# Kernel tuning notes

Hardware: AMD Instinct MI355X
Metric: run time of the kernel (lower is better)

Reference implementation:

```python
import jax, jax.numpy as jnp
import numpy as np

B, S, D, H = 2, 2048, 1024, 16
HD = D // H


def setup_inputs() -> dict:
    key = jax.random.key(0)
    ks = jax.random.split(key, 9)
    sc = 0.02
    return {
        "x": jax.random.normal(ks[0], (B, S, D), dtype=jnp.float32),
        "qw": jax.random.normal(ks[1], (D, D), dtype=jnp.float32) * sc,
        "qb": jax.random.normal(ks[2], (D,), dtype=jnp.float32) * sc,
        "kw": jax.random.normal(ks[3], (D, D), dtype=jnp.float32) * sc,
        "kb": jax.random.normal(ks[4], (D,), dtype=jnp.float32) * sc,
        "vw": jax.random.normal(ks[5], (D, D), dtype=jnp.float32) * sc,
        "vb": jax.random.normal(ks[6], (D,), dtype=jnp.float32) * sc,
        "ow": jax.random.normal(ks[7], (D, D), dtype=jnp.float32) * sc,
        "ob": jax.random.normal(ks[8], (D,), dtype=jnp.float32) * sc,
    }


def reference(x, qw, qb, kw, kb, vw, vb, ow, ob):
    b, s, d = x.shape
    # projections (torch Linear: x @ W.T + b)
    q = (x @ qw.T + qb).reshape(b, s, H, HD).transpose(0, 2, 1, 3)  # bhsd
    k = (x @ kw.T + kb).reshape(b, s, H, HD).transpose(0, 2, 1, 3)
    v = (x @ vw.T + vb).reshape(b, s, H, HD).transpose(0, 2, 1, 3)
    scale = 1.0 / jnp.sqrt(jnp.float32(HD))
    score = jnp.einsum("bhsd,bhtd->bhst", q, k) * scale  # bhss
    # causal mask: -inf strictly above diagonal
    mask = jnp.triu(jnp.full((s, s), -jnp.inf, dtype=score.dtype), k=1)
    score = jax.nn.softmax(score + mask, axis=-1)
    o = jnp.einsum("bhst,bhtd->bhsd", score, v)
    o = o.transpose(0, 2, 1, 3).reshape(b, s, d)
    return o @ ow.T + ob
```

## Files before the change

kernel.cpp:

```cpp
#include <hip/hip_runtime.h>
#include <hip/hip_bf16.h>
#include <stdint.h>

typedef __bf16 bf16x8 __attribute__((ext_vector_type(8)));
typedef __bf16 bf16x4 __attribute__((ext_vector_type(4)));
typedef float f32x4 __attribute__((ext_vector_type(4)));
typedef unsigned short ushort_t;


__device__ inline ushort_t f2bf(float f) {
  union { float f; uint32_t u; } v; v.f = f;
  uint32_t r = (v.u + 0x7fffu + ((v.u >> 16) & 1u)) >> 16;
  return (ushort_t)r;
}

__device__ inline void gll16(const void* g, void* l) {
  __builtin_amdgcn_global_load_lds((const __attribute__((address_space(1))) void*)g,
                                   (__attribute__((address_space(3))) void*)l, 16, 0, 0);
}

__global__ void cvt_x(const float* __restrict__ in, ushort_t* __restrict__ out) {
  int i = blockIdx.x * blockDim.x + threadIdx.x;
  float4 f = ((const float4*)in)[i];
  union { ushort_t u[4]; uint2 v; } r;
  r.u[0] = f2bf(f.x); r.u[1] = f2bf(f.y); r.u[2] = f2bf(f.z); r.u[3] = f2bf(f.w);
  ((uint2*)out)[i] = r.v;
}
__global__ void cvt_w(const float* __restrict__ a, const float* __restrict__ b,
                      const float* __restrict__ c, const float* __restrict__ d,
                      ushort_t* __restrict__ out) {
  const float* srcs[4] = {a, b, c, d};
  const float* s = srcs[blockIdx.y];
  ushort_t* o = out + (size_t)blockIdx.y * 1048576;
  int i = blockIdx.x * blockDim.x + threadIdx.x;
  float4 f = ((const float4*)s)[i];
  union { ushort_t u[4]; uint2 v; } r;
  r.u[0] = f2bf(f.x); r.u[1] = f2bf(f.y); r.u[2] = f2bf(f.z); r.u[3] = f2bf(f.w);
  ((uint2*)(o))[i] = r.v;
}

#define NKT 16

__device__ inline void stage_half(const ushort_t* __restrict__ g, ushort_t* l, int tid) {
  #pragma unroll
  for (int i = 0; i < 2; i++) {
    int c = tid + i * 512;
    int row = c >> 3;
    int q = (c & 7) ^ (row & 7);
    gll16(g + (size_t)row * 1024 + q * 8, l + c * 8);
  }
}

__global__ __launch_bounds__(512, 2) void qkv_gemm(
    const ushort_t* __restrict__ xb,
    const ushort_t* __restrict__ qwb, const ushort_t* __restrict__ kwb, const ushort_t* __restrict__ vwb,
    const float* __restrict__ qbias, const float* __restrict__ kbias, const float* __restrict__ vbias,
    ushort_t* __restrict__ qo, ushort_t* __restrict__ ko, ushort_t* __restrict__ vto)
{
  const int z = blockIdx.y;
  const int bx = blockIdx.x;
  const float* bias = (z == 0) ? qbias : (z == 1) ? kbias : vbias;
  const ushort_t* Ap;
  const ushort_t* Bp;
  int m0, n0;
  if (z == 2) {
    Ap = vwb; Bp = xb;
    m0 = (bx & 3) * 256;
    n0 = (bx >> 2) * 256;
  } else {
    Ap = xb; Bp = (z == 0) ? qwb : kwb;
    m0 = (bx >> 2) * 256;
    n0 = (bx & 3) * 256;
  }

  __shared__ __align__(16) ushort_t As[2][2][128 * 64];
  __shared__ __align__(16) ushort_t Bs[2][2][128 * 64];

  const int tid = threadIdx.x;
  const int w = tid >> 6;
  const int lane = tid & 63;
  const int ln = lane & 15;
  const int q4 = lane >> 4;
  const int wm = w & 1;
  const int wn = w >> 1;
  const int bh = wn >> 1;
  const int brow0 = (wn & 1) * 64;

  f32x4 acc[8][4];
  #pragma unroll
  for (int i = 0; i < 8; i++)
    #pragma unroll
    for (int j = 0; j < 4; j++) acc[i][j] = f32x4{0.f, 0.f, 0.f, 0.f};

  stage_half(Ap + (size_t)(m0 +   0) * 1024 +  0, &As[0][0][0], tid);
  stage_half(Ap + (size_t)(m0 + 128) * 1024 +  0, &As[0][1][0], tid);
  stage_half(Bp + (size_t)(n0 +   0) * 1024 +  0, &Bs[0][0][0], tid);
  stage_half(Bp + (size_t)(n0 + 128) * 1024 +  0, &Bs[0][1][0], tid);
  stage_half(Bp + (size_t)(n0 +   0) * 1024 + 64, &Bs[1][0][0], tid);
  stage_half(Bp + (size_t)(n0 + 128) * 1024 + 64, &Bs[1][1][0], tid);
  asm volatile("s_waitcnt vmcnt(4)" ::: "memory");
  __builtin_amdgcn_s_barrier();

  const int achk = ln & 7;

  for (int t = 0; t < NKT; ++t) {
    const int buf = t & 1;
    const ushort_t* Abuf = &As[buf][wm][0];
    const ushort_t* Bbuf = &Bs[buf][bh][0];

    bf16x8 a0[4][2], a4[4][2], b0[2][2], b2[2][2];

    #pragma unroll
    for (int m = 0; m < 4; m++)
      #pragma unroll
      for (int ks = 0; ks < 2; ks++)
        a0[m][ks] = *(const bf16x8*)&Abuf[(m * 16 + ln) * 64 + (((ks * 4 + q4) ^ achk) * 8)];
    #pragma unroll
    for (int n = 0; n < 2; n++)
      #pragma unroll
      for (int ks = 0; ks < 2; ks++)
        b0[n][ks] = *(const bf16x8*)&Bbuf[(brow0 + n * 16 + ln) * 64 + (((ks * 4 + q4) ^ achk) * 8)];
    if (t + 1 < NKT)
      stage_half(Ap + (size_t)m0 * 1024 + (t + 1) * 64, &As[(t + 1) & 1][0][0], tid);
    __builtin_amdgcn_s_barrier();
    asm volatile("s_waitcnt lgkmcnt(0)" ::: "memory");
    __builtin_amdgcn_s_setprio(1);
    #pragma unroll
    for (int m = 0; m < 4; m++)
      #pragma unroll
      for (int n = 0; n < 2; n++)
        #pragma unroll
        for (int ks = 0; ks < 2; ks++)
          acc[m][n] = __builtin_amdgcn_mfma_f32_16x16x32_bf16(a0[m][ks], b0[n][ks], acc[m][n], 0, 0, 0);
    __builtin_amdgcn_s_setprio(0);
    __builtin_amdgcn_s_barrier();

    #pragma unroll
    for (int n = 0; n < 2; n++)
      #pragma unroll
      for (int ks = 0; ks < 2; ks++)
        b2[n][ks] = *(const bf16x8*)&Bbuf[(brow0 + (n + 2) * 16 + ln) * 64 + (((ks * 4 + q4) ^ achk) * 8)];
    if (t + 1 < NKT)
      stage_half(Ap + (size_t)(m0 + 128) * 1024 + (t + 1) * 64, &As[(t + 1) & 1][1][0], tid);
    __builtin_amdgcn_s_barrier();
    asm volatile("s_waitcnt lgkmcnt(0)" ::: "memory");
    __builtin_amdgcn_s_setprio(1);
    #pragma unroll
    for (int m = 0; m < 4; m++)
      #pragma unroll
      for (int n = 0; n < 2; n++)
        #pragma unroll
        for (int ks = 0; ks < 2; ks++)
          acc[m][n + 2] = __builtin_amdgcn_mfma_f32_16x16x32_bf16(a0[m][ks], b2[n][ks], acc[m][n + 2], 0, 0, 0);
    __builtin_amdgcn_s_setprio(0);
    __builtin_amdgcn_s_barrier();

    #pragma unroll
    for (int m = 0; m < 4; m++)
      #pragma unroll
      for (int ks = 0; ks < 2; ks++)
        a4[m][ks] = *(const bf16x8*)&Abuf[((m + 4) * 16 + ln) * 64 + (((ks * 4 + q4) ^ achk) * 8)];
    if (t + 2 < NKT)
      stage_half(Bp + (size_t)n0 * 1024 + (t + 2) * 64, &Bs[buf][0][0], tid);
    __builtin_amdgcn_s_barrier();
    asm volatile("s_waitcnt lgkmcnt(0)" ::: "memory");
    __builtin_amdgcn_s_setprio(1);
    #pragma unroll
    for (int m = 0; m < 4; m++)
      #pragma unroll
      for (int n = 0; n < 2; n++)
        #pragma unroll
        for (int ks = 0; ks < 2; ks++)
          acc[m + 4][n + 2] = __builtin_amdgcn_mfma_f32_16x16x32_bf16(a4[m][ks], b2[n][ks], acc[m + 4][n + 2], 0, 0, 0);
    __builtin_amdgcn_s_setprio(0);
    __builtin_amdgcn_s_barrier();

    if (t + 2 < NKT)
      stage_half(Bp + (size_t)(n0 + 128) * 1024 + (t + 2) * 64, &Bs[buf][1][0], tid);
    __builtin_amdgcn_s_barrier();
    __builtin_amdgcn_s_setprio(1);
    #pragma unroll
    for (int m = 0; m < 4; m++)
      #pragma unroll
      for (int n = 0; n < 2; n++)
        #pragma unroll
        for (int ks = 0; ks < 2; ks++)
          acc[m + 4][n] = __builtin_amdgcn_mfma_f32_16x16x32_bf16(a4[m][ks], b0[n][ks], acc[m + 4][n], 0, 0, 0);
    __builtin_amdgcn_s_setprio(0);
    if (t + 2 < NKT) {
      asm volatile("s_waitcnt vmcnt(4)" ::: "memory");
    } else if (t + 1 < NKT) {
      asm volatile("s_waitcnt vmcnt(0)" ::: "memory");
    }
    __builtin_amdgcn_s_barrier();
  }

  if (z == 2) {
    #pragma unroll
    for (int n = 0; n < 4; n++) {
      int col = n0 + wn * 64 + n * 16 + ln;
      int bb = col >> 11, s = col & 2047;
      size_t base = (size_t)bb * 2097152 + s;
      #pragma unroll
      for (int m = 0; m < 8; m++) {
        int prow = m0 + wm * 128 + m * 16 + q4 * 4;
        #pragma unroll
        for (int r = 0; r < 4; r++) {
          int p = prow + r;
          vto[base + (size_t)p * 2048] = f2bf(acc[m][n][r] + bias[p]);
        }
      }
    }
  } else {
    #pragma unroll
    for (int n = 0; n < 4; n++) {
      int col = n0 + wn * 64 + n * 16 + ln;
      float bv = bias[col];
      int h = col >> 6, hd = col & 63;
      #pragma unroll
      for (int m = 0; m < 8; m++) {
        int rowb = m0 + wm * 128 + m * 16 + q4 * 4;
        #pragma unroll
        for (int r = 0; r < 4; r++) {
          int row = rowb + r;
          int b = row >> 11, s = row & 2047;
          float val = acc[m][n][r] + bv;
          if (z == 0) {
            qo[((size_t)((b * 16 + h) * 2048 + s)) * 64 + hd] = f2bf(val * 0.180336884f);
          } else {
            ko[((size_t)((b * 16 + h) * 2048 + s)) * 64 + hd] = f2bf(val);
          }
        }
      }
    }
  }
}

#define PAD 72
#define PPAD 68
__global__ __launch_bounds__(256) void attn(
    const ushort_t* __restrict__ qp, const ushort_t* __restrict__ kp,
    const ushort_t* __restrict__ vtp, ushort_t* __restrict__ op)
{
  __shared__ __align__(16) ushort_t Ks[64 * PAD];
  __shared__ __align__(16) ushort_t Vts[64 * PAD];
  __shared__ __align__(16) ushort_t Ps[8][16 * PPAD];

  const int tid = threadIdx.x;
  const int w = tid >> 6;
  const int lane = tid & 63;
  const int ln = lane & 15;
  const int q4 = lane >> 4;
  const int bh = blockIdx.y;
  const int b = bh >> 4, h = bh & 15;
  int tswz = (blockIdx.x + blockIdx.y) & 15;
  const int qt = (blockIdx.y & 16) ? (15 - tswz) : tswz;
  const int q0 = qt * 128;
  const int nt = 2 * qt + 2;

  const int c0 = tid, c1 = tid + 256;
  const int kr0_row = c0 >> 3, kr0_col = (c0 & 7) * 8;
  const int kr1_row = c1 >> 3, kr1_col = (c1 & 7) * 8;

  bf16x8 onesf;
  {
    union { ushort_t u[8]; bf16x8 v; } t;
    #pragma unroll
    for (int j = 0; j < 8; j++) t.u[j] = 0x3F80;
    onesf = t.v;
  }

  bf16x8 qf[2][2];
  #pragma unroll
  for (int s = 0; s < 2; s++) {
    const ushort_t* base = qp + ((size_t)bh * 2048 + q0 + w * 32 + s * 16 + ln) * 64 + q4 * 8;
    qf[s][0] = *(const bf16x8*)(base);
    qf[s][1] = *(const bf16x8*)(base + 32);
  }

  f32x4 acc_o[2][4];
  f32x4 acc_l[2];
  #pragma unroll
  for (int s = 0; s < 2; s++) {
    acc_l[s] = f32x4{0.f, 0.f, 0.f, 0.f};
    #pragma unroll
    for (int t = 0; t < 4; t++) acc_o[s][t] = f32x4{0.f, 0.f, 0.f, 0.f};
  }

  uint4 kr0, kr1, vr0, vr1;
  {
    const ushort_t* kb = kp + (size_t)bh * 2048 * 64;
    kr0 = *(const uint4*)(kb + kr0_row * 64 + kr0_col);
    kr1 = *(const uint4*)(kb + kr1_row * 64 + kr1_col);
    const ushort_t* vb = vtp + (size_t)bh * 64 * 2048;
    vr0 = *(const uint4*)(vb + (size_t)kr0_row * 2048 + kr0_col);
    vr1 = *(const uint4*)(vb + (size_t)kr1_row * 2048 + kr1_col);
  }

  for (int it = 0; it < nt; it++) {
    if (it) __syncthreads();
    *(uint4*)(&Ks [kr0_row * PAD + kr0_col]) = kr0;
    *(uint4*)(&Ks [kr1_row * PAD + kr1_col]) = kr1;
    *(uint4*)(&Vts[kr0_row * PAD + kr0_col]) = vr0;
    *(uint4*)(&Vts[kr1_row * PAD + kr1_col]) = vr1;
    __syncthreads();

    if (it + 1 < nt) {
      int kv1 = (it + 1) * 64;
      const ushort_t* kb = kp + ((size_t)bh * 2048 + kv1) * 64;
      kr0 = *(const uint4*)(kb + kr0_row * 64 + kr0_col);
      kr1 = *(const uint4*)(kb + kr1_row * 64 + kr1_col);
      const ushort_t* vb = vtp + (size_t)bh * 64 * 2048;
      vr0 = *(const uint4*)(vb + (size_t)kr0_row * 2048 + kv1 + kr0_col);
      vr1 = *(const uint4*)(vb + (size_t)kr1_row * 2048 + kv1 + kr1_col);
    }

    f32x4 sc[2][4];
    #pragma unroll
    for (int s = 0; s < 2; s++)
      #pragma unroll
      for (int t = 0; t < 4; t++) sc[s][t] = f32x4{0.f, 0.f, 0.f, 0.f};
    #pragma unroll
    for (int ks = 0; ks < 2; ks++) {
      bf16x8 kf[4];
      #pragma unroll
      for (int tn = 0; tn < 4; tn++)
        kf[tn] = *(const bf16x8*)(&Ks[(tn * 16 + ln) * PAD + ks * 32 + q4 * 8]);
      #pragma unroll
      for (int s = 0; s < 2; s++)
        #pragma unroll
        for (int tn = 0; tn < 4; tn++)
          sc[s][tn] = __builtin_amdgcn_mfma_f32_16x16x32_bf16(qf[s][ks], kf[tn], sc[s][tn], 0, 0, 0);
    }
    if (it >= 2 * qt) {
      int kv0 = it * 64;
      #pragma unroll
      for (int s = 0; s < 2; s++) {
        int qrow = q0 + w * 32 + s * 16 + q4 * 4;
        #pragma unroll
        for (int tn = 0; tn < 4; tn++) {
          int col = kv0 + tn * 16 + ln;
          #pragma unroll
          for (int r = 0; r < 4; r++)
            if (col > qrow + r) sc[s][tn][r] = -__builtin_inff();
        }
      }
    }
    #pragma unroll
    for (int s = 0; s < 2; s++)
      #pragma unroll
      for (int tn = 0; tn < 4; tn++)
        #pragma unroll
        for (int r = 0; r < 4; r++) {
          float p = __builtin_amdgcn_exp2f(sc[s][tn][r]);
          Ps[w * 2 + s][(q4 * 4 + r) * PPAD + tn * 16 + ln] = (ushort_t)(__float_as_uint(p) >> 16);
        }
    #pragma unroll
    for (int ks = 0; ks < 2; ks++) {
      bf16x8 vf[4];
      #pragma unroll
      for (int tn = 0; tn < 4; tn++)
        vf[tn] = *(const bf16x8*)(&Vts[(tn * 16 + ln) * PAD + ks * 32 + q4 * 8]);
      #pragma unroll
      for (int s = 0; s < 2; s++) {
        const ushort_t* pp = &Ps[w * 2 + s][ln * PPAD + ks * 32 + q4 * 8];
        bf16x4 plo = *(const bf16x4*)(pp);
        bf16x4 phi = *(const bf16x4*)(pp + 4);
        bf16x8 pf = __builtin_shufflevector(plo, phi, 0, 1, 2, 3, 4, 5, 6, 7);
        acc_l[s] = __builtin_amdgcn_mfma_f32_16x16x32_bf16(pf, onesf, acc_l[s], 0, 0, 0);
        #pragma unroll
        for (int tn = 0; tn < 4; tn++)
          acc_o[s][tn] = __builtin_amdgcn_mfma_f32_16x16x32_bf16(pf, vf[tn], acc_o[s][tn], 0, 0, 0);
      }
    }
  }

  #pragma unroll
  for (int s = 0; s < 2; s++) {
    float invl[4];
    #pragma unroll
    for (int r = 0; r < 4; r++) invl[r] = __builtin_amdgcn_rcpf(acc_l[s][r]);
    #pragma unroll
    for (int tn = 0; tn < 4; tn++)
      #pragma unroll
      for (int r = 0; r < 4; r++) {
        int row = q0 + w * 32 + s * 16 + q4 * 4 + r;
        op[((size_t)b * 2048 + row) * 1024 + h * 64 + tn * 16 + ln] =
            f2bf(acc_o[s][tn][r] * invl[r]);
      }
  }
}

__global__ __launch_bounds__(256) void out_gemm(
    const ushort_t* __restrict__ ob_in, const ushort_t* __restrict__ owb,
    const float* __restrict__ obias, float* __restrict__ out)
{
  __shared__ __align__(16) ushort_t As[64 * 64];
  __shared__ __align__(16) ushort_t Bs[128 * 64];

  const int tid = threadIdx.x;
  const int w = tid >> 6;
  const int lane = tid & 63;
  const int ln = lane & 15;
  const int q4 = lane >> 4;
  const int wm = w & 1, wn = w >> 1;
  const int m0 = blockIdx.y * 64;
  const int n0 = blockIdx.x * 128;

  f32x4 acc[2][4];
  #pragma unroll
  for (int i = 0; i < 2; i++)
    #pragma unroll
    for (int j = 0; j < 4; j++) acc[i][j] = f32x4{0.f, 0.f, 0.f, 0.f};

  for (int k0 = 0; k0 < 1024; k0 += 64) {
    __syncthreads();
    #pragma unroll
    for (int i = 0; i < 2; i++) {
      int c = tid + i * 256;
      int row = c >> 3;
      int cq = (c & 7) ^ (row & 7);
      gll16(&ob_in[(size_t)(m0 + row) * 1024 + k0 + cq * 8], &As[c * 8]);
    }
    #pragma unroll
    for (int i = 0; i < 4; i++) {
      int c = tid + i * 256;
      int row = c >> 3;
      int cq = (c & 7) ^ (row & 7);
      gll16(&owb[(size_t)(n0 + row) * 1024 + k0 + cq * 8], &Bs[c * 8]);
    }
    __syncthreads();
    #pragma unroll
    for (int ks = 0; ks < 2; ks++) {
      bf16x8 af[2], bfr[4];
      #pragma unroll
      for (int t = 0; t < 2; t++) {
        int rr = wm * 32 + t * 16 + ln;
        af[t] = *(const bf16x8*)(&As[rr * 64 + (((ks * 4 + q4) ^ (rr & 7)) * 8)]);
      }
      #pragma unroll
      for (int t = 0; t < 4; t++) {
        int rc = wn * 64 + t * 16 + ln;
        bfr[t] = *(const bf16x8*)(&Bs[rc * 64 + (((ks * 4 + q4) ^ (rc & 7)) * 8)]);
      }
      #pragma unroll
      for (int tm = 0; tm < 2; tm++)
        #pragma unroll
        for (int tn = 0; tn < 4; tn++)
          acc[tm][tn] = __builtin_amdgcn_mfma_f32_16x16x32_bf16(af[tm], bfr[tn], acc[tm][tn], 0, 0, 0);
    }
  }

  #pragma unroll
  for (int tn = 0; tn < 4; tn++) {
    int col = n0 + wn * 64 + tn * 16 + ln;
    float bv = obias[col];
    #pragma unroll
    for (int tm = 0; tm < 2; tm++) {
      int rowb = m0 + wm * 32 + tm * 16 + q4 * 4;
      #pragma unroll
      for (int r = 0; r < 4; r++)
        out[(size_t)(rowb + r) * 1024 + col] = acc[tm][tn][r] + bv;
    }
  }
}

extern "C" void kernel_launch(void* const* d_in, const int* in_sizes, int n_in,
                              void* d_out, int out_size, void* d_ws, size_t ws_size,
                              hipStream_t stream) {
  const float* x     = (const float*)d_in[0];
  const float* qw    = (const float*)d_in[1];
  const float* qb    = (const float*)d_in[2];
  const float* kw    = (const float*)d_in[3];
  const float* kb    = (const float*)d_in[4];
  const float* vw    = (const float*)d_in[5];
  const float* vb    = (const float*)d_in[6];
  const float* ow    = (const float*)d_in[7];
  const float* obias = (const float*)d_in[8];
  float* out = (float*)d_out;

  char* ws = (char*)d_ws;
  ushort_t* xb  = (ushort_t*)(ws);
  ushort_t* wb  = (ushort_t*)(ws + 8388608);
  ushort_t* qwb = wb;
  ushort_t* kwb = wb + 1048576;
  ushort_t* vwb = wb + 2097152;
  ushort_t* owb = wb + 3145728;
  ushort_t* qo  = (ushort_t*)(ws + 16777216);
  ushort_t* ko  = (ushort_t*)(ws + 25165824);
  ushort_t* vto = (ushort_t*)(ws + 33554432);
  ushort_t* oo  = (ushort_t*)(ws + 41943040);

  cvt_x<<<dim3(4096), dim3(256), 0, stream>>>(x, xb);
  cvt_w<<<dim3(1024, 4), dim3(256), 0, stream>>>(qw, kw, vw, ow, wb);

  qkv_gemm<<<dim3(64, 3), dim3(512), 0, stream>>>(xb, qwb, kwb, vwb, qb, kb, vb, qo, ko, vto);
  attn<<<dim3(16, 32), dim3(256), 0, stream>>>(qo, ko, vto, oo);
  out_gemm<<<dim3(8, 64), dim3(256), 0, stream>>>(oo, owb, obias, out);
}
```

Measured before the change: 184.9 us.

## Double-buffer attention K/V, keep P in registers, triple-buffer out-projection GEMM

The attention kernel now double-buffers K/V tiles in shared memory with a two-step-ahead register prefetch, so there is one barrier per iteration. It computes scores transposed so the exp'd probabilities can be packed with v_cvt_pk_bf16 and redistributed with ds_bpermute instead of a round trip through an LDS P buffer. MFMA phases are wrapped in s_setprio. The output GEMM gets a 3-stage global_load_lds pipeline with explicit vmcnt waits, which raises LDS use per block and relies on exact outstanding-load counts for correctness.

```diff
diff --git a/kernel.cpp b/kernel.cpp
--- a/kernel.cpp
+++ b/kernel.cpp
@@ -12,6 +12,12 @@
   union { float f; uint32_t u; } v; v.f = f;
   uint32_t r = (v.u + 0x7fffu + ((v.u >> 16) & 1u)) >> 16;
   return (ushort_t)r;
+}
+
+__device__ inline uint32_t cvtpk_bf16(float lo, float hi) {
+  uint32_t r;
+  asm("v_cvt_pk_bf16_f32 %0, %1, %2" : "=v"(r) : "v"(lo), "v"(hi));
+  return r;
 }
 
 __device__ inline void gll16(const void* g, void* l) {
@@ -237,20 +243,21 @@
 }
 
 #define PAD 72
-#define PPAD 68
 __global__ __launch_bounds__(256) void attn(
     const ushort_t* __restrict__ qp, const ushort_t* __restrict__ kp,
     const ushort_t* __restrict__ vtp, ushort_t* __restrict__ op)
 {
-  __shared__ __align__(16) ushort_t Ks[64 * PAD];
-  __shared__ __align__(16) ushort_t Vts[64 * PAD];
-  __shared__ __align__(16) ushort_t Ps[8][16 * PPAD];
+  __shared__ __align__(16) ushort_t Ks[2][64 * PAD];
+  __shared__ __align__(16) ushort_t Vts[2][64 * PAD];
 
   const int tid = threadIdx.x;
   const int w = tid >> 6;
   const int lane = tid & 63;
   const int ln = lane & 15;
   const int q4 = lane >> 4;
+  const bool alo = (q4 < 2);
+  const int psel0 = (((q4 & 1) * 32) + ln) << 2;
+  const int psel1 = psel0 + (16 << 2);
   const int bh = blockIdx.y;
   const int b = bh >> 4, h = bh & 15;
   int tswz = (blockIdx.x + blockIdx.y) & 15;
@@ -287,32 +294,39 @@
     for (int t = 0; t < 4; t++) acc_o[s][t] = f32x4{0.f, 0.f, 0.f, 0.f};
   }
 
+  const ushort_t* kb = kp + (size_t)bh * 2048 * 64;
+  const ushort_t* vb = vtp + (size_t)bh * 64 * 2048;
+
   uint4 kr0, kr1, vr0, vr1;
-  {
-    const ushort_t* kb = kp + (size_t)bh * 2048 * 64;
-    kr0 = *(const uint4*)(kb + kr0_row * 64 + kr0_col);
-    kr1 = *(const uint4*)(kb + kr1_row * 64 + kr1_col);
-    const ushort_t* vb = vtp + (size_t)bh * 64 * 2048;
-    vr0 = *(const uint4*)(vb + (size_t)kr0_row * 2048 + kr0_col);
-    vr1 = *(const uint4*)(vb + (size_t)kr1_row * 2048 + kr1_col);
-  }
+  kr0 = *(const uint4*)(kb + kr0_row * 64 + kr0_col);
+  kr1 = *(const uint4*)(kb + kr1_row * 64 + kr1_col);
+  vr0 = *(const uint4*)(vb + (size_t)kr0_row * 2048 + kr0_col);
+  vr1 = *(const uint4*)(vb + (size_t)kr1_row * 2048 + kr1_col);
+  *(uint4*)(&Ks [0][kr0_row * PAD + kr0_col]) = kr0;
+  *(uint4*)(&Ks [0][kr1_row * PAD + kr1_col]) = kr1;
+  *(uint4*)(&Vts[0][kr0_row * PAD + kr0_col]) = vr0;
+  *(uint4*)(&Vts[0][kr1_row * PAD + kr1_col]) = vr1;
+  kr0 = *(const uint4*)(kb + 64 * 64 + kr0_row * 64 + kr0_col);
+  kr1 = *(const uint4*)(kb + 64 * 64 + kr1_row * 64 + kr1_col);
+  vr0 = *(const uint4*)(vb + (size_t)kr0_row * 2048 + 64 + kr0_col);
+  vr1 = *(const uint4*)(vb + (size_t)kr1_row * 2048 + 64 + kr1_col);
 
   for (int it = 0; it < nt; it++) {
-    if (it) __syncthreads();
-    *(uint4*)(&Ks [kr0_row * PAD + kr0_col]) = kr0;
-    *(uint4*)(&Ks [kr1_row * PAD + kr1_col]) = kr1;
-    *(uint4*)(&Vts[kr0_row * PAD + kr0_col]) = vr0;
-    *(uint4*)(&Vts[kr1_row * PAD + kr1_col]) = vr1;
+    const int cur = it & 1;
     __syncthreads();
-
     if (it + 1 < nt) {
-      int kv1 = (it + 1) * 64;
-      const ushort_t* kb = kp + ((size_t)bh * 2048 + kv1) * 64;
-      kr0 = *(const uint4*)(kb + kr0_row * 64 + kr0_col);
-      kr1 = *(const uint4*)(kb + kr1_row * 64 + kr1_col);
-      const ushort_t* vb = vtp + (size_t)bh * 64 * 2048;
-      vr0 = *(const uint4*)(vb + (size_t)kr0_row * 2048 + kv1 + kr0_col);
-      vr1 = *(const uint4*)(vb + (size_t)kr1_row * 2048 + kv1 + kr1_col);
+      const int nxt = cur ^ 1;
+      *(uint4*)(&Ks [nxt][kr0_row * PAD + kr0_col]) = kr0;
+      *(uint4*)(&Ks [nxt][kr1_row * PAD + kr1_col]) = kr1;
+      *(uint4*)(&Vts[nxt][kr0_row * PAD + kr0_col]) = vr0;
+      *(uint4*)(&Vts[nxt][kr1_row * PAD + kr1_col]) = vr1;
+    }
+    if (it + 2 < nt) {
+      int kv2 = (it + 2) * 64;
+      kr0 = *(const uint4*)(kb + (size_t)kv2 * 64 + kr0_row * 64 + kr0_col);
+      kr1 = *(const uint4*)(kb + (size_t)kv2 * 64 + kr1_row * 64 + kr1_col);
+      vr0 = *(const uint4*)(vb + (size_t)kr0_row * 2048 + kv2 + kr0_col);
+      vr1 = *(const uint4*)(vb + (size_t)kr1_row * 2048 + kv2 + kr1_col);
     }
 
     f32x4 sc[2][4];
@@ -320,59 +334,82 @@
     for (int s = 0; s < 2; s++)
       #pragma unroll
       for (int t = 0; t < 4; t++) sc[s][t] = f32x4{0.f, 0.f, 0.f, 0.f};
+    __builtin_amdgcn_s_setprio(1);
     #pragma unroll
     for (int ks = 0; ks < 2; ks++) {
       bf16x8 kf[4];
       #pragma unroll
       for (int tn = 0; tn < 4; tn++)
-        kf[tn] = *(const bf16x8*)(&Ks[(tn * 16 + ln) * PAD + ks * 32 + q4 * 8]);
+        kf[tn] = *(const bf16x8*)(&Ks[cur][(tn * 16 + ln) * PAD + ks * 32 + q4 * 8]);
       #pragma unroll
       for (int s = 0; s < 2; s++)
         #pragma unroll
         for (int tn = 0; tn < 4; tn++)
-          sc[s][tn] = __builtin_amdgcn_mfma_f32_16x16x32_bf16(qf[s][ks], kf[tn], sc[s][tn], 0, 0, 0);
-    }
+          sc[s][tn] = __builtin_amdgcn_mfma_f32_16x16x32_bf16(kf[tn], qf[s][ks], sc[s][tn], 0, 0, 0);
+    }
+    __builtin_amdgcn_s_setprio(0);
+
     if (it >= 2 * qt) {
-      int kv0 = it * 64;
       #pragma unroll
       for (int s = 0; s < 2; s++) {
-        int qrow = q0 + w * 32 + s * 16 + q4 * 4;
+        int qrow = q0 + w * 32 + s * 16 + ln;
         #pragma unroll
         for (int tn = 0; tn < 4; tn++) {
-          int col = kv0 + tn * 16 + ln;
+          int kvb = it * 64 + tn * 16 + q4 * 4;
           #pragma unroll
           for (int r = 0; r < 4; r++)
-            if (col > qrow + r) sc[s][tn][r] = -__builtin_inff();
+            if (kvb + r > qrow) sc[s][tn][r] = -__builtin_inff();
         }
       }
     }
+
+    uint32_t pw[2][4][2];
     #pragma unroll
     for (int s = 0; s < 2; s++)
       #pragma unroll
       for (int tn = 0; tn < 4; tn++)
         #pragma unroll
-        for (int r = 0; r < 4; r++) {
-          float p = __builtin_amdgcn_exp2f(sc[s][tn][r]);
-          Ps[w * 2 + s][(q4 * 4 + r) * PPAD + tn * 16 + ln] = (ushort_t)(__float_as_uint(p) >> 16);
+        for (int rh = 0; rh < 2; rh++) {
+          float lo = __builtin_amdgcn_exp2f(sc[s][tn][2 * rh]);
+          float hi = __builtin_amdgcn_exp2f(sc[s][tn][2 * rh + 1]);
+          pw[s][tn][rh] = cvtpk_bf16(lo, hi);
         }
+    uint32_t pfw[2][2][4];
+    #pragma unroll
+    for (int s = 0; s < 2; s++)
+      #pragma unroll
+      for (int ks = 0; ks < 2; ks++)
+        #pragma unroll
+        for (int rh = 0; rh < 2; rh++) {
+          int a  = (int)pw[s][2 * ks][rh];
+          int bb = (int)pw[s][2 * ks + 1][rh];
+          int A0 = __builtin_amdgcn_ds_bpermute(psel0, a);
+          int B0 = __builtin_amdgcn_ds_bpermute(psel0, bb);
+          int A1 = __builtin_amdgcn_ds_bpermute(psel1, a);
+          int B1 = __builtin_amdgcn_ds_bpermute(psel1, bb);
+          pfw[s][ks][rh]     = (uint32_t)(alo ? A0 : B0);
+          pfw[s][ks][2 + rh] = (uint32_t)(alo ? A1 : B1);
+        }
+
+    __builtin_amdgcn_s_setprio(1);
     #pragma unroll
     for (int ks = 0; ks < 2; ks++) {
       bf16x8 vf[4];
       #pragma unroll
       for (int tn = 0; tn < 4; tn++)
-        vf[tn] = *(const bf16x8*)(&Vts[(tn * 16 + ln) * PAD + ks * 32 + q4 * 8]);
+        vf[tn] = *(const bf16x8*)(&Vts[cur][(tn * 16 + ln) * PAD + ks * 32 + q4 * 8]);
       #pragma unroll
       for (int s = 0; s < 2; s++) {
-        const ushort_t* pp = &Ps[w * 2 + s][ln * PPAD + ks * 32 + q4 * 8];
-        bf16x4 plo = *(const bf16x4*)(pp);
-        bf16x4 phi = *(const bf16x4*)(pp + 4);
-        bf16x8 pf = __builtin_shufflevector(plo, phi, 0, 1, 2, 3, 4, 5, 6, 7);
-        acc_l[s] = __builtin_amdgcn_mfma_f32_16x16x32_bf16(pf, onesf, acc_l[s], 0, 0, 0);
+        union { uint32_t u[4]; bf16x8 v; } U;
+        #pragma unroll
+        for (int wi = 0; wi < 4; wi++) U.u[wi] = pfw[s][ks][wi];
+        acc_l[s] = __builtin_amdgcn_mfma_f32_16x16x32_bf16(U.v, onesf, acc_l[s], 0, 0, 0);
         #pragma unroll
         for (int tn = 0; tn < 4; tn++)
-          acc_o[s][tn] = __builtin_amdgcn_mfma_f32_16x16x32_bf16(pf, vf[tn], acc_o[s][tn], 0, 0, 0);
-      }
-    }
+          acc_o[s][tn] = __builtin_amdgcn_mfma_f32_16x16x32_bf16(U.v, vf[tn], acc_o[s][tn], 0, 0, 0);
+      }
+    }
+    __builtin_amdgcn_s_setprio(0);
   }
 
   #pragma unroll
@@ -395,8 +432,8 @@
     const ushort_t* __restrict__ ob_in, const ushort_t* __restrict__ owb,
     const float* __restrict__ obias, float* __restrict__ out)
 {
-  __shared__ __align__(16) ushort_t As[64 * 64];
-  __shared__ __align__(16) ushort_t Bs[128 * 64];
+  __shared__ __align__(16) ushort_t As[3][64 * 64];
+  __shared__ __align__(16) ushort_t Bs[3][128 * 64];
 
   const int tid = threadIdx.x;
   const int w = tid >> 6;
@@ -413,35 +450,44 @@
     #pragma unroll
     for (int j = 0; j < 4; j++) acc[i][j] = f32x4{0.f, 0.f, 0.f, 0.f};
 
-  for (int k0 = 0; k0 < 1024; k0 += 64) {
-    __syncthreads();
+  auto STAGE = [&](int bi, int k0) {
     #pragma unroll
     for (int i = 0; i < 2; i++) {
       int c = tid + i * 256;
       int row = c >> 3;
       int cq = (c & 7) ^ (row & 7);
-      gll16(&ob_in[(size_t)(m0 + row) * 1024 + k0 + cq * 8], &As[c * 8]);
+      gll16(&ob_in[(size_t)(m0 + row) * 1024 + k0 + cq * 8], &As[bi][c * 8]);
     }
     #pragma unroll
     for (int i = 0; i < 4; i++) {
       int c = tid + i * 256;
       int row = c >> 3;
       int cq = (c & 7) ^ (row & 7);
-      gll16(&owb[(size_t)(n0 + row) * 1024 + k0 + cq * 8], &Bs[c * 8]);
-    }
-    __syncthreads();
+      gll16(&owb[(size_t)(n0 + row) * 1024 + k0 + cq * 8], &Bs[bi][c * 8]);
+    }
+  };
+
+  STAGE(0, 0);
+  STAGE(1, 64);
+  asm volatile("s_waitcnt vmcnt(6)" ::: "memory");
+  __builtin_amdgcn_s_barrier();
+
+  #pragma unroll
+  for (int t = 0; t < 16; t++) {
+    const int cb = t % 3;
+    if (t + 2 < 16) STAGE((t + 2) % 3, (t + 2) * 64);
     #pragma unroll
     for (int ks = 0; ks < 2; ks++) {
       bf16x8 af[2], bfr[4];
       #pragma unroll
-      for (int t = 0; t < 2; t++) {
-        int rr = wm * 32 + t * 16 + ln;
-        af[t] = *(const bf16x8*)(&As[rr * 64 + (((ks * 4 + q4) ^ (rr & 7)) * 8)]);
-      }
-      #pragma unroll
-      for (int t = 0; t < 4; t++) {
-        int rc = wn * 64 + t * 16 + ln;
-        bfr[t] = *(const bf16x8*)(&Bs[rc * 64 + (((ks * 4 + q4) ^ (rc & 7)) * 8)]);
+      for (int tt = 0; tt < 2; tt++) {
+        int rr = wm * 32 + tt * 16 + ln;
+        af[tt] = *(const bf16x8*)(&As[cb][rr * 64 + (((ks * 4 + q4) ^ (rr & 7)) * 8)]);
+      }
+      #pragma unroll
+      for (int tt = 0; tt < 4; tt++) {
+        int rc = wn * 64 + tt * 16 + ln;
+        bfr[tt] = *(const bf16x8*)(&Bs[cb][rc * 64 + (((ks * 4 + q4) ^ (rc & 7)) * 8)]);
       }
       #pragma unroll
       for (int tm = 0; tm < 2; tm++)
@@ -449,6 +495,12 @@
         for (int tn = 0; tn < 4; tn++)
           acc[tm][tn] = __builtin_amdgcn_mfma_f32_16x16x32_bf16(af[tm], bfr[tn], acc[tm][tn], 0, 0, 0);
     }
+    if (t + 2 < 16) {
+      asm volatile("s_waitcnt vmcnt(6)" ::: "memory");
+    } else if (t + 1 < 16) {
+      asm volatile("s_waitcnt vmcnt(0)" ::: "memory");
+    }
+    __builtin_amdgcn_s_barrier();
   }
 
   #pragma unroll
```

Result: slower. 189.6 us (+2.5%).

## Halve attention query tile, add MFMA priority, triple-buffer output GEMM loads

Applied to the files above, without the earlier changes.

The attention kernel now gives each block 64 query rows instead of 128, with one 16-row slice per wave and twice as many blocks. The aim is better occupancy and finer causal load balance, at the cost of reloading K/V tiles twice as often per query. It also raises wave priority around the MFMA sections. The output projection GEMM moves to a three-stage async global-to-LDS pipeline with explicit vmcnt waits, so tile loads overlap compute, at the cost of three times the shared memory.

```diff
diff --git a/kernel.cpp b/kernel.cpp
--- a/kernel.cpp
+++ b/kernel.cpp
@@ -244,7 +244,7 @@
 {
   __shared__ __align__(16) ushort_t Ks[64 * PAD];
   __shared__ __align__(16) ushort_t Vts[64 * PAD];
-  __shared__ __align__(16) ushort_t Ps[8][16 * PPAD];
+  __shared__ __align__(16) ushort_t Ps[4][16 * PPAD];
 
   const int tid = threadIdx.x;
   const int w = tid >> 6;
@@ -253,10 +253,10 @@
   const int q4 = lane >> 4;
   const int bh = blockIdx.y;
   const int b = bh >> 4, h = bh & 15;
-  int tswz = (blockIdx.x + blockIdx.y) & 15;
-  const int qt = (blockIdx.y & 16) ? (15 - tswz) : tswz;
-  const int q0 = qt * 128;
-  const int nt = 2 * qt + 2;
+  int tswz = (blockIdx.x + blockIdx.y) & 31;
+  const int qt = (blockIdx.y & 16) ? (31 - tswz) : tswz;
+  const int q0 = qt * 64;
+  const int nt = qt + 1;
 
   const int c0 = tid, c1 = tid + 256;
   const int kr0_row = c0 >> 3, kr0_col = (c0 & 7) * 8;
@@ -270,32 +270,26 @@
     onesf = t.v;
   }
 
-  bf16x8 qf[2][2];
-  #pragma unroll
-  for (int s = 0; s < 2; s++) {
-    const ushort_t* base = qp + ((size_t)bh * 2048 + q0 + w * 32 + s * 16 + ln) * 64 + q4 * 8;
-    qf[s][0] = *(const bf16x8*)(base);
-    qf[s][1] = *(const bf16x8*)(base + 32);
-  }
-
-  f32x4 acc_o[2][4];
-  f32x4 acc_l[2];
-  #pragma unroll
-  for (int s = 0; s < 2; s++) {
-    acc_l[s] = f32x4{0.f, 0.f, 0.f, 0.f};
-    #pragma unroll
-    for (int t = 0; t < 4; t++) acc_o[s][t] = f32x4{0.f, 0.f, 0.f, 0.f};
-  }
+  bf16x8 qf[2];
+  {
+    const ushort_t* base = qp + ((size_t)bh * 2048 + q0 + w * 16 + ln) * 64 + q4 * 8;
+    qf[0] = *(const bf16x8*)(base);
+    qf[1] = *(const bf16x8*)(base + 32);
+  }
+
+  f32x4 acc_o[4];
+  f32x4 acc_l = f32x4{0.f, 0.f, 0.f, 0.f};
+  #pragma unroll
+  for (int t = 0; t < 4; t++) acc_o[t] = f32x4{0.f, 0.f, 0.f, 0.f};
+
+  const ushort_t* kb = kp + (size_t)bh * 2048 * 64;
+  const ushort_t* vb = vtp + (size_t)bh * 64 * 2048;
 
   uint4 kr0, kr1, vr0, vr1;
-  {
-    const ushort_t* kb = kp + (size_t)bh * 2048 * 64;
-    kr0 = *(const uint4*)(kb + kr0_row * 64 + kr0_col);
-    kr1 = *(const uint4*)(kb + kr1_row * 64 + kr1_col);
-    const ushort_t* vb = vtp + (size_t)bh * 64 * 2048;
-    vr0 = *(const uint4*)(vb + (size_t)kr0_row * 2048 + kr0_col);
-    vr1 = *(const uint4*)(vb + (size_t)kr1_row * 2048 + kr1_col);
-  }
+  kr0 = *(const uint4*)(kb + kr0_row * 64 + kr0_col);
+  kr1 = *(const uint4*)(kb + kr1_row * 64 + kr1_col);
+  vr0 = *(const uint4*)(vb + (size_t)kr0_row * 2048 + kr0_col);
+  vr1 = *(const uint4*)(vb + (size_t)kr1_row * 2048 + kr1_col);
 
   for (int it = 0; it < nt; it++) {
     if (it) __syncthreads();
@@ -307,19 +301,16 @@
 
     if (it + 1 < nt) {
       int kv1 = (it + 1) * 64;
-      const ushort_t* kb = kp + ((size_t)bh * 2048 + kv1) * 64;
-      kr0 = *(const uint4*)(kb + kr0_row * 64 + kr0_col);
-      kr1 = *(const uint4*)(kb + kr1_row * 64 + kr1_col);
-      const ushort_t* vb = vtp + (size_t)bh * 64 * 2048;
+      kr0 = *(const uint4*)(kb + (size_t)kv1 * 64 + kr0_row * 64 + kr0_col);
+      kr1 = *(const uint4*)(kb + (size_t)kv1 * 64 + kr1_row * 64 + kr1_col);
       vr0 = *(const uint4*)(vb + (size_t)kr0_row * 2048 + kv1 + kr0_col);
       vr1 = *(const uint4*)(vb + (size_t)kr1_row * 2048 + kv1 + kr1_col);
     }
 
-    f32x4 sc[2][4];
-    #pragma unroll
-    for (int s = 0; s < 2; s++)
-      #pragma unroll
-      for (int t = 0; t < 4; t++) sc[s][t] = f32x4{0.f, 0.f, 0.f, 0.f};
+    f32x4 sc[4];
+    #pragma unroll
+    for (int t = 0; t < 4; t++) sc[t] = f32x4{0.f, 0.f, 0.f, 0.f};
+    __builtin_amdgcn_s_setprio(1);
     #pragma unroll
     for (int ks = 0; ks < 2; ks++) {
       bf16x8 kf[4];
@@ -327,66 +318,58 @@
       for (int tn = 0; tn < 4; tn++)
         kf[tn] = *(const bf16x8*)(&Ks[(tn * 16 + ln) * PAD + ks * 32 + q4 * 8]);
       #pragma unroll
-      for (int s = 0; s < 2; s++)
-        #pragma unroll
-        for (int tn = 0; tn < 4; tn++)
-          sc[s][tn] = __builtin_amdgcn_mfma_f32_16x16x32_bf16(qf[s][ks], kf[tn], sc[s][tn], 0, 0, 0);
-    }
-    if (it >= 2 * qt) {
-      int kv0 = it * 64;
-      #pragma unroll
-      for (int s = 0; s < 2; s++) {
-        int qrow = q0 + w * 32 + s * 16 + q4 * 4;
-        #pragma unroll
-        for (int tn = 0; tn < 4; tn++) {
-          int col = kv0 + tn * 16 + ln;
-          #pragma unroll
-          for (int r = 0; r < 4; r++)
-            if (col > qrow + r) sc[s][tn][r] = -__builtin_inff();
-        }
-      }
-    }
-    #pragma unroll
-    for (int s = 0; s < 2; s++)
-      #pragma unroll
       for (int tn = 0; tn < 4; tn++)
-        #pragma unroll
-        for (int r = 0; r < 4; r++) {
-          float p = __builtin_amdgcn_exp2f(sc[s][tn][r]);
-          Ps[w * 2 + s][(q4 * 4 + r) * PPAD + tn * 16 + ln] = (ushort_t)(__float_as_uint(p) >> 16);
-        }
+        sc[tn] = __builtin_amdgcn_mfma_f32_16x16x32_bf16(qf[ks], kf[tn], sc[tn], 0, 0, 0);
+    }
+    __builtin_amdgcn_s_setprio(0);
+
+    if (it == qt) {
+      int qrow = w * 16 + q4 * 4;
+      #pragma unroll
+      for (int tn = 0; tn < 4; tn++) {
+        int col = tn * 16 + ln;
+        #pragma unroll
+        for (int r = 0; r < 4; r++)
+          if (col > qrow + r) sc[tn][r] = -__builtin_inff();
+      }
+    }
+    #pragma unroll
+    for (int tn = 0; tn < 4; tn++)
+      #pragma unroll
+      for (int r = 0; r < 4; r++) {
+        float p = __builtin_amdgcn_exp2f(sc[tn][r]);
+        Ps[w][(q4 * 4 + r) * PPAD + tn * 16 + ln] = (ushort_t)(__float_as_uint(p) >> 16);
+      }
+    __builtin_amdgcn_s_setprio(1);
     #pragma unroll
     for (int ks = 0; ks < 2; ks++) {
       bf16x8 vf[4];
       #pragma unroll
       for (int tn = 0; tn < 4; tn++)
         vf[tn] = *(const bf16x8*)(&Vts[(tn * 16 + ln) * PAD + ks * 32 + q4 * 8]);
-      #pragma unroll
-      for (int s = 0; s < 2; s++) {
-        const ushort_t* pp = &Ps[w * 2 + s][ln * PPAD + ks * 32 + q4 * 8];
-        bf16x4 plo = *(const bf16x4*)(pp);
-        bf16x4 phi = *(const bf16x4*)(pp + 4);
-        bf16x8 pf = __builtin_shufflevector(plo, phi, 0, 1, 2, 3, 4, 5, 6, 7);
-        acc_l[s] = __builtin_amdgcn_mfma_f32_16x16x32_bf16(pf, onesf, acc_l[s], 0, 0, 0);
-        #pragma unroll
-        for (int tn = 0; tn < 4; tn++)
-          acc_o[s][tn] = __builtin_amdgcn_mfma_f32_16x16x32_bf16(pf, vf[tn], acc_o[s][tn], 0, 0, 0);
-      }
-    }
-  }
-
-  #pragma unroll
-  for (int s = 0; s < 2; s++) {
+      const ushort_t* pp = &Ps[w][ln * PPAD + ks * 32 + q4 * 8];
+      bf16x4 plo = *(const bf16x4*)(pp);
+      bf16x4 phi = *(const bf16x4*)(pp + 4);
+      bf16x8 pf = __builtin_shufflevector(plo, phi, 0, 1, 2, 3, 4, 5, 6, 7);
+      acc_l = __builtin_amdgcn_mfma_f32_16x16x32_bf16(pf, onesf, acc_l, 0, 0, 0);
+      #pragma unroll
+      for (int tn = 0; tn < 4; tn++)
+        acc_o[tn] = __builtin_amdgcn_mfma_f32_16x16x32_bf16(pf, vf[tn], acc_o[tn], 0, 0, 0);
+    }
+    __builtin_amdgcn_s_setprio(0);
+  }
+
+  {
     float invl[4];
     #pragma unroll
-    for (int r = 0; r < 4; r++) invl[r] = __builtin_amdgcn_rcpf(acc_l[s][r]);
+    for (int r = 0; r < 4; r++) invl[r] = __builtin_amdgcn_rcpf(acc_l[r]);
     #pragma unroll
     for (int tn = 0; tn < 4; tn++)
       #pragma unroll
       for (int r = 0; r < 4; r++) {
-        int row = q0 + w * 32 + s * 16 + q4 * 4 + r;
+        int row = q0 + w * 16 + q4 * 4 + r;
         op[((size_t)b * 2048 + row) * 1024 + h * 64 + tn * 16 + ln] =
-            f2bf(acc_o[s][tn][r] * invl[r]);
+            f2bf(acc_o[tn][r] * invl[r]);
       }
   }
 }
@@ -395,8 +378,8 @@
     const ushort_t* __restrict__ ob_in, const ushort_t* __restrict__ owb,
     const float* __restrict__ obias, float* __restrict__ out)
 {
-  __shared__ __align__(16) ushort_t As[64 * 64];
-  __shared__ __align__(16) ushort_t Bs[128 * 64];
+  __shared__ __align__(16) ushort_t As[3][64 * 64];
+  __shared__ __align__(16) ushort_t Bs[3][128 * 64];
 
   const int tid = threadIdx.x;
   const int w = tid >> 6;
@@ -413,35 +396,44 @@
     #pragma unroll
     for (int j = 0; j < 4; j++) acc[i][j] = f32x4{0.f, 0.f, 0.f, 0.f};
 
-  for (int k0 = 0; k0 < 1024; k0 += 64) {
-    __syncthreads();
+  auto STAGE = [&](int bi, int k0) {
     #pragma unroll
     for (int i = 0; i < 2; i++) {
       int c = tid + i * 256;
       int row = c >> 3;
       int cq = (c & 7) ^ (row & 7);
-      gll16(&ob_in[(size_t)(m0 + row) * 1024 + k0 + cq * 8], &As[c * 8]);
+      gll16(&ob_in[(size_t)(m0 + row) * 1024 + k0 + cq * 8], &As[bi][c * 8]);
     }
     #pragma unroll
     for (int i = 0; i < 4; i++) {
       int c = tid + i * 256;
       int row = c >> 3;
       int cq = (c & 7) ^ (row & 7);
-      gll16(&owb[(size_t)(n0 + row) * 1024 + k0 + cq * 8], &Bs[c * 8]);
-    }
-    __syncthreads();
+      gll16(&owb[(size_t)(n0 + row) * 1024 + k0 + cq * 8], &Bs[bi][c * 8]);
+    }
+  };
+
+  STAGE(0, 0);
+  STAGE(1, 64);
+  asm volatile("s_waitcnt vmcnt(6)" ::: "memory");
+  __builtin_amdgcn_s_barrier();
+
+  #pragma unroll
+  for (int t = 0; t < 16; t++) {
+    const int cb = t % 3;
+    if (t + 2 < 16) STAGE((t + 2) % 3, (t + 2) * 64);
     #pragma unroll
     for (int ks = 0; ks < 2; ks++) {
       bf16x8 af[2], bfr[4];
       #pragma unroll
-      for (int t = 0; t < 2; t++) {
-        int rr = wm * 32 + t * 16 + ln;
-        af[t] = *(const bf16x8*)(&As[rr * 64 + (((ks * 4 + q4) ^ (rr & 7)) * 8)]);
-      }
-      #pragma unroll
-      for (int t = 0; t < 4; t++) {
-        int rc = wn * 64 + t * 16 + ln;
-        bfr[t] = *(const bf16x8*)(&Bs[rc * 64 + (((ks * 4 + q4) ^ (rc & 7)) * 8)]);
+      for (int tt = 0; tt < 2; tt++) {
+        int rr = wm * 32 + tt * 16 + ln;
+        af[tt] = *(const bf16x8*)(&As[cb][rr * 64 + (((ks * 4 + q4) ^ (rr & 7)) * 8)]);
+      }
+      #pragma unroll
+      for (int tt = 0; tt < 4; tt++) {
+        int rc = wn * 64 + tt * 16 + ln;
+        bfr[tt] = *(const bf16x8*)(&Bs[cb][rc * 64 + (((ks * 4 + q4) ^ (rc & 7)) * 8)]);
       }
       #pragma unroll
       for (int tm = 0; tm < 2; tm++)
@@ -449,6 +441,12 @@
         for (int tn = 0; tn < 4; tn++)
           acc[tm][tn] = __builtin_amdgcn_mfma_f32_16x16x32_bf16(af[tm], bfr[tn], acc[tm][tn], 0, 0, 0);
     }
+    if (t + 2 < 16) {
+      asm volatile("s_waitcnt vmcnt(6)" ::: "memory");
+    } else if (t + 1 < 16) {
+      asm volatile("s_waitcnt vmcnt(0)" ::: "memory");
+    }
+    __builtin_amdgcn_s_barrier();
   }
 
   #pragma unroll
@@ -495,6 +493,6 @@
   cvt_w<<<dim3(1024, 4), dim3(256), 0, stream>>>(qw, kw, vw, ow, wb);
 
   qkv_gemm<<<dim3(64, 3), dim3(512), 0, stream>>>(xb, qwb, kwb, vwb, qb, kb, vb, qo, ko, vto);
-  attn<<<dim3(16, 32), dim3(256), 0, stream>>>(qo, ko, vto, oo);
+  attn<<<dim3(32, 32), dim3(256), 0, stream>>>(qo, ko, vto, oo);
   out_gemm<<<dim3(8, 64), dim3(256), 0, stream>>>(oo, owb, obias, out);
 }
```

Result: slower. 193.5 us (+4.6%).
